# Performance work log

Hardware: AMD Instinct MI355X
Metric: run time of the kernel (lower is better)

Reference implementation:

```python
import jax, jax.numpy as jnp
import numpy as np

B = 4194304  # number of sequential rows


def setup_inputs() -> dict:
    key = jax.random.key(0)
    k1, k2, k3, k4 = jax.random.split(key, 4)
    x = jax.random.normal(k1, (B, 1, 3), dtype=jnp.float32)
    # nn.Linear(3, 3) params
    lim = 1.0 / np.sqrt(3.0)
    W = jax.random.uniform(k2, (3, 3), minval=-lim, maxval=lim, dtype=jnp.float32)
    b = jax.random.uniform(k3, (3,), minval=-lim, maxval=lim, dtype=jnp.float32)
    # FastNetwork init: (-1-1)*rand([3,1]) + 1  -> uniform in [-1, 1]
    net0 = jax.random.uniform(k4, (3, 1), minval=-1.0, maxval=1.0, dtype=jnp.float32)
    return {"x": x, "W": W, "b": b, "net0": net0}


def reference(x, W, b, net0):
    # x: [B,1,3]; W: [3,3]; b: [3]; net0: [3,1]
    xi = x[:, 0, :]                      # [B,3]
    # Updater: per-row Linear(3,3) -- batched as one matmul
    updates = xi @ W.T + b               # [B,3]

    def step(net, inp):
        x_row, u = inp                   # x_row: [3], u: [3]
        # 1/(1+exp(-10*(net + update - 0.5))) == sigmoid(10*(net + update - 0.5))
        net = jax.nn.sigmoid(10.0 * (net + u[:, None] - 0.5))  # [3,1]
        pred = x_row @ net               # [1]
        return net, pred

    _, preds = jax.lax.scan(step, net0, (xi, updates))
    return preds                         # [B,1]
```

## Files before the change

### kernel.cpp

```cpp
#include <hip/hip_runtime.h>


#if __has_builtin(__builtin_amdgcn_exp2f)
#define EXP2F(v) __builtin_amdgcn_exp2f(v)
#else
#define EXP2F(v) __expf(0.6931471805599453f * (v))
#endif

namespace {
constexpr int   BTOT   = 4194304;
constexpr int   CHUNK  = 16;
constexpr int   BLOCK  = 256;
constexpr int   BSTEPS = BLOCK * CHUNK;
constexpr int   WARM   = 32;
constexpr int   GRID   = BTOT / BSTEPS;
constexpr int   LDSF   = (BSTEPS + WARM) * 3;
constexpr float KEXP   = -14.426950408889634f;
constexpr float EPS    = 1e-6f;
}

#define CVALS(X0, X1, X2)                                                     \
  const float c0 = fmaf(kw00, (X0), fmaf(kw01, (X1), fmaf(kw02, (X2), kb0)));  \
  const float c1 = fmaf(kw10, (X0), fmaf(kw11, (X1), fmaf(kw12, (X2), kb1)));  \
  const float c2 = fmaf(kw20, (X0), fmaf(kw21, (X1), fmaf(kw22, (X2), kb2)));

#define SIG(N, C) __builtin_amdgcn_rcpf(1.0f + EXP2F(fmaf(KEXP, (N), (C))))

#define US(X0, X1, X2)                                                        \
  do {                                                                        \
    CVALS(X0, X1, X2)                                                         \
    lo0 = SIG(lo0, c0); hi0 = SIG(hi0, c0);                                   \
    lo1 = SIG(lo1, c1); hi1 = SIG(hi1, c1);                                   \
    lo2 = SIG(lo2, c2); hi2 = SIG(hi2, c2);                                   \
  } while (0)

#define SS(X0, X1, X2)                                                        \
  do {                                                                        \
    CVALS(X0, X1, X2)                                                         \
    m0 = SIG(m0, c0); m1 = SIG(m1, c1); m2 = SIG(m2, c2);                     \
  } while (0)

#define MS(IDX, X0, X1, X2)                                                   \
  do {                                                                        \
    CVALS(X0, X1, X2)                                                         \
    m0 = SIG(m0, c0); m1 = SIG(m1, c1); m2 = SIG(m2, c2);                     \
    pr[(IDX)] = fmaf((X0), m0, fmaf((X1), m1, (X2) * m2));                    \
  } while (0)

__global__ __launch_bounds__(BLOCK) void Updater_65395172049297_kernel(
    const float* __restrict__ x, const float* __restrict__ W,
    const float* __restrict__ bv, const float* __restrict__ n0v,
    float* __restrict__ out)
{
    __shared__ float lds[LDSF];

    const float kw00 = KEXP * W[0], kw01 = KEXP * W[1], kw02 = KEXP * W[2];
    const float kw10 = KEXP * W[3], kw11 = KEXP * W[4], kw12 = KEXP * W[5];
    const float kw20 = KEXP * W[6], kw21 = KEXP * W[7], kw22 = KEXP * W[8];
    const float kb0 = KEXP * (bv[0] - 0.5f);
    const float kb1 = KEXP * (bv[1] - 0.5f);
    const float kb2 = KEXP * (bv[2] - 0.5f);
    const float n00 = n0v[0], n01 = n0v[1], n02 = n0v[2];

    const long S = (long)blockIdx.x * BSTEPS;
    if (blockIdx.x == 0) {
        const float4* src = reinterpret_cast<const float4*>(x);
        float4*       dst = reinterpret_cast<float4*>(lds + WARM * 3);
        for (int i = threadIdx.x; i < BSTEPS * 3 / 4; i += BLOCK) dst[i] = src[i];
    } else {
        const float4* src = reinterpret_cast<const float4*>(x + 3 * (S - WARM));
        float4*       dst = reinterpret_cast<float4*>(lds);
        for (int i = threadIdx.x; i < LDSF / 4; i += BLOCK) dst[i] = src[i];
    }
    __syncthreads();

    const int  t     = threadIdx.x;
    const long start = S + (long)t * CHUNK;
    const int  wl    = (int)((start < (long)WARM) ? start : (long)WARM);
    const bool exact = (start - wl) == 0;
    const int  gw    = wl >> 2;
    const int  lbeg  = (int)(start - S + WARM) * 3 - wl * 3;

    float lo0, lo1, lo2, hi0, hi1, hi2, m0, m1, m2;
    bool  conv = false;
    int   g    = 0;

    if (exact) {
        m0 = n00; m1 = n01; m2 = n02; conv = true;
    } else {
        lo0 = lo1 = lo2 = 0.0f; hi0 = hi1 = hi2 = 1.0f;
        for (; g < gw; ) {
            const float4* p = reinterpret_cast<const float4*>(&lds[lbeg + 12 * g]);
            const float4 a = p[0], b4 = p[1], c4 = p[2];
            US(a.x, a.y, a.z);
            US(a.w, b4.x, b4.y);
            US(b4.z, b4.w, c4.x);
            US(c4.y, c4.z, c4.w);
            ++g;
            conv = ((hi0 - lo0) < EPS) & ((hi1 - lo1) < EPS) & ((hi2 - lo2) < EPS);
            if (__all(conv)) break;
        }
        if (conv) { m0 = 0.5f * (lo0 + hi0); m1 = 0.5f * (lo1 + hi1); m2 = 0.5f * (lo2 + hi2); }
    }

    if (conv) {
        for (; g < gw; ++g) {
            const float4* p = reinterpret_cast<const float4*>(&lds[lbeg + 12 * g]);
            const float4 a = p[0], b4 = p[1], c4 = p[2];
            SS(a.x, a.y, a.z);
            SS(a.w, b4.x, b4.y);
            SS(b4.z, b4.w, c4.x);
            SS(c4.y, c4.z, c4.w);
        }
    } else {
        for (int a = 1; a < 10 && !conv; ++a) {
            long wl2 = (long)WARM << (2 * a);
            long bgn = start - wl2;
            bool ex2 = (bgn <= 0);
            if (ex2) bgn = 0;
            if (ex2) { lo0 = hi0 = n00; lo1 = hi1 = n01; lo2 = hi2 = n02; }
            else     { lo0 = lo1 = lo2 = 0.0f; hi0 = hi1 = hi2 = 1.0f; }
            for (long s2 = bgn; s2 < start; ++s2) {
                const float X0 = x[3 * s2], X1 = x[3 * s2 + 1], X2 = x[3 * s2 + 2];
                US(X0, X1, X2);
            }
            conv = ex2 || (((hi0 - lo0) < EPS) & ((hi1 - lo1) < EPS) & ((hi2 - lo2) < EPS));
        }
        m0 = 0.5f * (lo0 + hi0); m1 = 0.5f * (lo1 + hi1); m2 = 0.5f * (lo2 + hi2);
    }

    const int lm = (int)(start - S + WARM) * 3;
    float pr[CHUNK];
#pragma unroll
    for (int q = 0; q < CHUNK / 4; ++q) {
        const float4* p = reinterpret_cast<const float4*>(&lds[lm + 12 * q]);
        const float4 a = p[0], b4 = p[1], c4 = p[2];
        MS(4 * q + 0, a.x, a.y, a.z);
        MS(4 * q + 1, a.w, b4.x, b4.y);
        MS(4 * q + 2, b4.z, b4.w, c4.x);
        MS(4 * q + 3, c4.y, c4.z, c4.w);
    }

    float4* op = reinterpret_cast<float4*>(out + start);
#pragma unroll
    for (int i = 0; i < CHUNK / 4; ++i)
        op[i] = make_float4(pr[4 * i + 0], pr[4 * i + 1], pr[4 * i + 2], pr[4 * i + 3]);
}

extern "C" void kernel_launch(void* const* d_in, const int* in_sizes, int n_in,
                              void* d_out, int out_size, void* d_ws, size_t ws_size,
                              hipStream_t stream) {
    const float* x   = (const float*)d_in[0];
    const float* W   = (const float*)d_in[1];
    const float* bv  = (const float*)d_in[2];
    const float* n0v = (const float*)d_in[3];
    float*       out = (float*)d_out;
    Updater_65395172049297_kernel<<<GRID, BLOCK, 0, stream>>>(x, W, bv, n0v, out);
}
```

Baseline: 101.0 us.

## Load warmup and chunk inputs directly into registers, dropping the LDS staging

Removes the shared-memory staging and the block barrier. Each thread now loads its warmup window and its own chunk of x straight from global memory into float4 register arrays, with half the chunk prefetched before the warmup and the rest loaded afterwards. The warmup window shrinks from 32 to 16 steps, the fallback retry limit rises, and launch bounds now request 4 blocks per SM. The per-thread float4 loads are strided across threads rather than coalesced, and the register arrays add pressure. The shorter warmup may send more threads into the slow global-memory fallback path.

```diff
diff --git a/kernel.cpp b/kernel.cpp
--- a/kernel.cpp
+++ b/kernel.cpp
@@ -8,51 +8,76 @@
 #endif
 
 namespace {
-constexpr int   BTOT   = 4194304;
-constexpr int   CHUNK  = 16;
-constexpr int   BLOCK  = 256;
-constexpr int   BSTEPS = BLOCK * CHUNK;
-constexpr int   WARM   = 32;
-constexpr int   GRID   = BTOT / BSTEPS;
-constexpr int   LDSF   = (BSTEPS + WARM) * 3;
-constexpr float KEXP   = -14.426950408889634f;
-constexpr float EPS    = 1e-6f;
+constexpr int   BTOT  = 4194304;
+constexpr int   CHUNK = 16;
+constexpr int   BLOCK = 256;
+constexpr int   WARM  = 16;
+constexpr int   NTHR  = BTOT / CHUNK;
+constexpr int   GRID  = NTHR / BLOCK;
+constexpr float KEXP  = -14.426950408889634f;
+constexpr float EPS   = 1e-6f;
 }
 
-#define CVALS(X0, X1, X2)                                                     \
+#define CVALS(X0, X1, X2)                                                      \
   const float c0 = fmaf(kw00, (X0), fmaf(kw01, (X1), fmaf(kw02, (X2), kb0)));  \
   const float c1 = fmaf(kw10, (X0), fmaf(kw11, (X1), fmaf(kw12, (X2), kb1)));  \
   const float c2 = fmaf(kw20, (X0), fmaf(kw21, (X1), fmaf(kw22, (X2), kb2)));
 
 #define SIG(N, C) __builtin_amdgcn_rcpf(1.0f + EXP2F(fmaf(KEXP, (N), (C))))
 
-#define US(X0, X1, X2)                                                        \
-  do {                                                                        \
-    CVALS(X0, X1, X2)                                                         \
-    lo0 = SIG(lo0, c0); hi0 = SIG(hi0, c0);                                   \
-    lo1 = SIG(lo1, c1); hi1 = SIG(hi1, c1);                                   \
-    lo2 = SIG(lo2, c2); hi2 = SIG(hi2, c2);                                   \
+#define US(X0, X1, X2)                                                         \
+  do {                                                                         \
+    CVALS(X0, X1, X2)                                                          \
+    lo0 = SIG(lo0, c0); hi0 = SIG(hi0, c0);                                    \
+    lo1 = SIG(lo1, c1); hi1 = SIG(hi1, c1);                                    \
+    lo2 = SIG(lo2, c2); hi2 = SIG(hi2, c2);                                    \
   } while (0)
 
-#define SS(X0, X1, X2)                                                        \
-  do {                                                                        \
-    CVALS(X0, X1, X2)                                                         \
-    m0 = SIG(m0, c0); m1 = SIG(m1, c1); m2 = SIG(m2, c2);                     \
+#define SS(X0, X1, X2)                                                         \
+  do {                                                                         \
+    CVALS(X0, X1, X2)                                                          \
+    m0 = SIG(m0, c0); m1 = SIG(m1, c1); m2 = SIG(m2, c2);                      \
   } while (0)
 
-#define MS(IDX, X0, X1, X2)                                                   \
-  do {                                                                        \
-    CVALS(X0, X1, X2)                                                         \
-    m0 = SIG(m0, c0); m1 = SIG(m1, c1); m2 = SIG(m2, c2);                     \
-    pr[(IDX)] = fmaf((X0), m0, fmaf((X1), m1, (X2) * m2));                    \
+#define MS(IDX, X0, X1, X2)                                                    \
+  do {                                                                         \
+    CVALS(X0, X1, X2)                                                          \
+    m0 = SIG(m0, c0); m1 = SIG(m1, c1); m2 = SIG(m2, c2);                      \
+    pr[(IDX)] = fmaf((X0), m0, fmaf((X1), m1, (X2) * m2));                     \
   } while (0)
 
-__global__ __launch_bounds__(BLOCK) void Updater_65395172049297_kernel(
+#define US4(A, B4, C4)                                                         \
+  do { US((A).x,(A).y,(A).z); US((A).w,(B4).x,(B4).y);                         \
+       US((B4).z,(B4).w,(C4).x); US((C4).y,(C4).z,(C4).w); } while (0)
+#define SS4(A, B4, C4)                                                         \
+  do { SS((A).x,(A).y,(A).z); SS((A).w,(B4).x,(B4).y);                         \
+       SS((B4).z,(B4).w,(C4).x); SS((C4).y,(C4).z,(C4).w); } while (0)
+#define MS4(Q, A, B4, C4)                                                      \
+  do { MS(4*(Q)+0,(A).x,(A).y,(A).z); MS(4*(Q)+1,(A).w,(B4).x,(B4).y);         \
+       MS(4*(Q)+2,(B4).z,(B4).w,(C4).x); MS(4*(Q)+3,(C4).y,(C4).z,(C4).w); } while (0)
+
+__global__ __launch_bounds__(BLOCK, 4) void Updater_65395172049297_kernel(
     const float* __restrict__ x, const float* __restrict__ W,
     const float* __restrict__ bv, const float* __restrict__ n0v,
     float* __restrict__ out)
 {
-    __shared__ float lds[LDSF];
+    const int  tid   = blockIdx.x * BLOCK + threadIdx.x;
+    const long start = (long)tid * CHUNK;
+
+    const int  wl    = (start < (long)WARM) ? (int)start : WARM;
+    const bool exact = (start == (long)wl);
+    const int  gw    = wl >> 2;
+
+    const float4* wp = reinterpret_cast<const float4*>(x + 3 * (start - wl));
+    const float4* xp = reinterpret_cast<const float4*>(x + 3 * start);
+    float4 wb[12];
+    if (gw) {
+#pragma unroll
+        for (int i = 0; i < 12; ++i) wb[i] = wp[i];
+    }
+    float4 mb[12];
+#pragma unroll
+    for (int i = 0; i < 6; ++i) mb[i] = xp[i];
 
     const float kw00 = KEXP * W[0], kw01 = KEXP * W[1], kw02 = KEXP * W[2];
     const float kw10 = KEXP * W[3], kw11 = KEXP * W[4], kw12 = KEXP * W[5];
@@ -61,25 +86,6 @@
     const float kb1 = KEXP * (bv[1] - 0.5f);
     const float kb2 = KEXP * (bv[2] - 0.5f);
     const float n00 = n0v[0], n01 = n0v[1], n02 = n0v[2];
-
-    const long S = (long)blockIdx.x * BSTEPS;
-    if (blockIdx.x == 0) {
-        const float4* src = reinterpret_cast<const float4*>(x);
-        float4*       dst = reinterpret_cast<float4*>(lds + WARM * 3);
-        for (int i = threadIdx.x; i < BSTEPS * 3 / 4; i += BLOCK) dst[i] = src[i];
-    } else {
-        const float4* src = reinterpret_cast<const float4*>(x + 3 * (S - WARM));
-        float4*       dst = reinterpret_cast<float4*>(lds);
-        for (int i = threadIdx.x; i < LDSF / 4; i += BLOCK) dst[i] = src[i];
-    }
-    __syncthreads();
-
-    const int  t     = threadIdx.x;
-    const long start = S + (long)t * CHUNK;
-    const int  wl    = (int)((start < (long)WARM) ? start : (long)WARM);
-    const bool exact = (start - wl) == 0;
-    const int  gw    = wl >> 2;
-    const int  lbeg  = (int)(start - S + WARM) * 3 - wl * 3;
 
     float lo0, lo1, lo2, hi0, hi1, hi2, m0, m1, m2;
     bool  conv = false;
@@ -90,30 +96,18 @@
     } else {
         lo0 = lo1 = lo2 = 0.0f; hi0 = hi1 = hi2 = 1.0f;
         for (; g < gw; ) {
-            const float4* p = reinterpret_cast<const float4*>(&lds[lbeg + 12 * g]);
-            const float4 a = p[0], b4 = p[1], c4 = p[2];
-            US(a.x, a.y, a.z);
-            US(a.w, b4.x, b4.y);
-            US(b4.z, b4.w, c4.x);
-            US(c4.y, c4.z, c4.w);
+            US4(wb[3*g], wb[3*g+1], wb[3*g+2]);
             ++g;
             conv = ((hi0 - lo0) < EPS) & ((hi1 - lo1) < EPS) & ((hi2 - lo2) < EPS);
             if (__all(conv)) break;
         }
-        if (conv) { m0 = 0.5f * (lo0 + hi0); m1 = 0.5f * (lo1 + hi1); m2 = 0.5f * (lo2 + hi2); }
+        if (conv) { m0 = 0.5f*(lo0+hi0); m1 = 0.5f*(lo1+hi1); m2 = 0.5f*(lo2+hi2); }
     }
 
     if (conv) {
-        for (; g < gw; ++g) {
-            const float4* p = reinterpret_cast<const float4*>(&lds[lbeg + 12 * g]);
-            const float4 a = p[0], b4 = p[1], c4 = p[2];
-            SS(a.x, a.y, a.z);
-            SS(a.w, b4.x, b4.y);
-            SS(b4.z, b4.w, c4.x);
-            SS(c4.y, c4.z, c4.w);
-        }
+        for (; g < gw; ++g) SS4(wb[3*g], wb[3*g+1], wb[3*g+2]);
     } else {
-        for (int a = 1; a < 10 && !conv; ++a) {
+        for (int a = 1; a < 12 && !conv; ++a) {
             long wl2 = (long)WARM << (2 * a);
             long bgn = start - wl2;
             bool ex2 = (bgn <= 0);
@@ -121,30 +115,28 @@
             if (ex2) { lo0 = hi0 = n00; lo1 = hi1 = n01; lo2 = hi2 = n02; }
             else     { lo0 = lo1 = lo2 = 0.0f; hi0 = hi1 = hi2 = 1.0f; }
             for (long s2 = bgn; s2 < start; ++s2) {
-                const float X0 = x[3 * s2], X1 = x[3 * s2 + 1], X2 = x[3 * s2 + 2];
+                const float X0 = x[3*s2], X1 = x[3*s2+1], X2 = x[3*s2+2];
                 US(X0, X1, X2);
             }
-            conv = ex2 || (((hi0 - lo0) < EPS) & ((hi1 - lo1) < EPS) & ((hi2 - lo2) < EPS));
+            conv = ex2 || (((hi0 - lo0) < EPS) & ((hi1 - lo1) < EPS) &
+                           ((hi2 - lo2) < EPS));
         }
-        m0 = 0.5f * (lo0 + hi0); m1 = 0.5f * (lo1 + hi1); m2 = 0.5f * (lo2 + hi2);
+        m0 = 0.5f*(lo0+hi0); m1 = 0.5f*(lo1+hi1); m2 = 0.5f*(lo2+hi2);
     }
 
-    const int lm = (int)(start - S + WARM) * 3;
+#pragma unroll
+    for (int i = 6; i < 12; ++i) mb[i] = xp[i];
+
     float pr[CHUNK];
-#pragma unroll
-    for (int q = 0; q < CHUNK / 4; ++q) {
-        const float4* p = reinterpret_cast<const float4*>(&lds[lm + 12 * q]);
-        const float4 a = p[0], b4 = p[1], c4 = p[2];
-        MS(4 * q + 0, a.x, a.y, a.z);
-        MS(4 * q + 1, a.w, b4.x, b4.y);
-        MS(4 * q + 2, b4.z, b4.w, c4.x);
-        MS(4 * q + 3, c4.y, c4.z, c4.w);
-    }
+    MS4(0, mb[0], mb[1],  mb[2]);
+    MS4(1, mb[3], mb[4],  mb[5]);
+    MS4(2, mb[6], mb[7],  mb[8]);
+    MS4(3, mb[9], mb[10], mb[11]);
 
     float4* op = reinterpret_cast<float4*>(out + start);
 #pragma unroll
     for (int i = 0; i < CHUNK / 4; ++i)
-        op[i] = make_float4(pr[4 * i + 0], pr[4 * i + 1], pr[4 * i + 2], pr[4 * i + 3]);
+        op[i] = make_float4(pr[4*i+0], pr[4*i+1], pr[4*i+2], pr[4*i+3]);
 }
 
 extern "C" void kernel_launch(void* const* d_in, const int* in_sizes, int n_in,
```

After: 138.6 us. 1.37x slower.
